# Optimization experiments

Hardware: AMD Instinct MI355X
Metric: run time of the kernel (lower is better)

## Reference

```python
import jax, jax.numpy as jnp
import numpy as np

EPS = 1e-5
B, L, D_MSA, D_PAIR = 1, 512, 256, 128
D_STATE, L0_IN, L0_OUT, EF = 32, 32, 32, 32
CV_IN, CV_OUT, C_HID = 3, 3, 32
TOP_K = 64
D_NODE_IN = D_MSA + 21 + D_STATE  # 309
D_INV = 2 * L0_IN + EF + 1 + CV_IN  # 100


def ln(x, g, b):
    mu = x.mean(-1, keepdims=True)
    var = ((x - mu) ** 2).mean(-1, keepdims=True)
    return (x - mu) * jax.lax.rsqrt(var + EPS) * g + b


def setup_inputs():
    key = jax.random.key(0)
    ks = iter(jax.random.split(key, 64))
    r = lambda *s: jax.random.normal(next(ks), s, jnp.float32)
    inp = {
        'xyz': r(B, L, 3, 3) * 3.0,
        'state': r(B, L, D_STATE),
        'atom_coor': r(B, L, 14, 3),
        'atom_feat': r(B, L, 14, 21),
        'msa': r(B, L, D_MSA),
        'pair': r(B, L, L, D_PAIR),
        'seq1hot': jax.random.uniform(next(ks), (B, L, 21)),
        'idx': jnp.arange(L, dtype=jnp.int32)[None].repeat(B, 0),
        'CA_atom_index': jax.random.randint(next(ks), (B, L), 0, 14),
        'top_k': TOP_K,
        # LayerNorm params
        'g_msa': jnp.ones(D_MSA), 'b_msa': jnp.zeros(D_MSA),
        'g_pair': jnp.ones(D_PAIR), 'b_pair': jnp.zeros(D_PAIR),
        'g_state': jnp.ones(D_STATE), 'b_state': jnp.zeros(D_STATE),
        'g_node': jnp.ones(L0_IN), 'b_node': jnp.zeros(L0_IN),
        'g_e1': jnp.ones(EF), 'b_e1': jnp.zeros(EF),
        # embeddings
        'Wx': r(D_NODE_IN, L0_IN) * 0.02, 'bx': jnp.zeros(L0_IN),
        'We1': r(D_PAIR, EF) * 0.02, 'be1': jnp.zeros(EF),
        # SE3-equivariant layer params
        'W1': r(D_INV, C_HID) * 0.1, 'b1': jnp.zeros(C_HID),
        'W2': r(L0_IN + C_HID, L0_OUT) * 0.1, 'b2': jnp.zeros(L0_OUT),
        'Wv': r(C_HID, 2 * CV_OUT) * 0.1,
        'Wvv': r(CV_IN, CV_OUT) * 0.3,
        'Wself': r(CV_IN, CV_OUT) * 0.3,
        # lddt head
        'Wl': r(L0_OUT, 1) * 0.1, 'bl': jnp.zeros(1),
    }
    return inp


def reference(xyz, state, atom_coor, atom_feat, msa, pair, seq1hot, idx,
              CA_atom_index, top_k, g_msa, b_msa, g_pair, b_pair, g_state,
              b_state, g_node, b_node, g_e1, b_e1, Wx, bx, We1, be1,
              W1, b1, W2, b2, Wv, Wvv, Wself, Wl, bl):
    Bb, Ll = msa.shape[:2]
    N = Bb * Ll
    # node / pair / state embeddings with fused LN+Linear chains
    node = ln(msa, g_msa, b_msa)
    pair_n = ln(pair, g_pair, b_pair)
    st = ln(state, g_state, b_state)
    node = jnp.concatenate([node, seq1hot, st], axis=-1)          # [B,L,309]
    node = ln(node @ Wx + bx, g_node, b_node)                      # [B,L,32]
    pair_e = ln(pair_n @ We1 + be1, g_e1, b_e1)                    # [B,L,L,32]

    # ---- make_graph_topk: kNN graph on CA coords ----
    CA = xyz[:, :, 1]                                              # [B,L,3]
    D = jnp.sqrt(jnp.sum((CA[:, :, None] - CA[:, None]) ** 2, -1) + 1e-8)
    D = D + 999.9 * jnp.eye(Ll, dtype=D.dtype)
    _, nbr = jax.lax.top_k(-D, top_k)                              # [B,L,k]
    src = jnp.repeat(jnp.arange(N), top_k)                         # [E]
    dst = (nbr + (jnp.arange(Bb) * Ll)[:, None, None]).reshape(-1) # [E]
    CAf = CA.reshape(N, 3)
    d_e = jax.lax.stop_gradient(CAf[dst] - CAf[src])               # [E,3] (detached as in torch)
    w_e = jnp.take_along_axis(pair_e.reshape(N, Ll, EF),
                              nbr.reshape(N, top_k, 1), axis=1).reshape(-1, EF)

    # ---- SE(3)-equivariant message passing (degree-0 + degree-1) ----
    l0 = node.reshape(N, -1)                                       # [N,32]
    v = (xyz - CA[:, :, None]).reshape(N, CV_IN, 3)                # [N,3,3]
    dn = jnp.linalg.norm(d_e, axis=-1, keepdims=True)              # [E,1]
    du = d_e / (dn + 1e-8)
    sv = jnp.einsum('eiv,ev->ei', v[src], du)                      # [E,3] invariants
    inv = jnp.concatenate([l0[src], l0[dst], w_e, dn, sv], -1)     # [E,100]
    m = jax.nn.gelu(inv @ W1 + b1)                                 # [E,32]
    agg = jax.ops.segment_sum(m, dst, num_segments=N)              # [N,32] scatter
    h_out = jnp.concatenate([l0, agg], -1) @ W2 + b2               # [N,32]
    coef = m @ Wv                                                  # [E,6]
    cd, cv = coef[:, :CV_OUT], coef[:, CV_OUT:]
    vproj = jnp.einsum('io,niv->nov', Wvv, v)                      # [N,3,3]
    vmsg = cd[:, :, None] * d_e[:, None] + cv[:, :, None] * vproj[src]
    v_agg = jax.ops.segment_sum(vmsg, dst, num_segments=N)         # [N,3,3]
    v_out = jnp.einsum('io,niv->nov', Wself, v) + v_agg            # [N,3,3]

    # ---- assemble refined coordinates ----
    state_o = h_out.reshape(Bb, Ll, -1)
    offset = v_out.reshape(Bb, Ll, -1, 3)
    CA_new = CA + offset[:, :, 1]
    CA_set = jnp.repeat(CA_new[:, :, None], 3, axis=2)
    CA_set = CA_set.at[:, 0:1].set(0.0)
    xyz_new = (offset + CA_set).reshape(Bb * Ll * 3, 3)
    lddt = jax.nn.sigmoid(ln(state_o, g_state, b_state) @ Wl + bl)
    return xyz_new, lddt
```

## Files before the change

### kernel.cpp

```cpp
#include <hip/hip_runtime.h>
#include <hip/hip_bf16.h>
#include <math.h>

typedef __hip_bfloat16 bf16;

__device__ __forceinline__ bool detect_bf16(const void* ones_vec) {
  return ((const unsigned int*)ones_vec)[0] == 0x3F803F80u;
}
__device__ __forceinline__ float ldf(const void* p, long idx, bool isb) {
  if (isb) return __bfloat162float(((const bf16*)p)[idx]);
  return ((const float*)p)[idx];
}
__device__ __forceinline__ void stf(void* p, long idx, float v, bool isb) {
  if (isb) ((bf16*)p)[idx] = __float2bfloat16(v);
  else     ((float*)p)[idx] = v;
}
__device__ __forceinline__ float wsum64(float x) {
#pragma unroll
  for (int off = 32; off > 0; off >>= 1) x += __shfl_xor(x, off, 64);
  return x;
}
__device__ __forceinline__ float wsum32(float x) {
#pragma unroll
  for (int off = 16; off > 0; off >>= 1) x += __shfl_xor(x, off, 64);
  return x;
}

__global__ __launch_bounds__(256) void k_node_topk(
    const void* __restrict__ xyz, const void* __restrict__ state,
    const void* __restrict__ msa, const void* __restrict__ seq1hot,
    const void* __restrict__ g_msa, const void* __restrict__ b_msa,
    const void* __restrict__ g_state, const void* __restrict__ b_state,
    const void* __restrict__ g_node, const void* __restrict__ b_node,
    const void* __restrict__ Wx, const void* __restrict__ bx,
    const void* __restrict__ Wvv,
    float* __restrict__ l0, float* __restrict__ CA, float* __restrict__ v,
    float* __restrict__ vproj, float* __restrict__ agg, float* __restrict__ v_agg,
    int* __restrict__ nbr)
{
  const bool isb = detect_bf16(g_msa);
  const int i = blockIdx.x;
  const int t = threadIdx.x;
  const int lane = t & 63, w = t >> 6;
  __shared__ float nin[312];
  __shared__ float wred[2][4];
  __shared__ float part[8][32];
  __shared__ float sxyz[9], sv9[9];
  __shared__ float cx[512], cy[512], cz[512];
  __shared__ unsigned long long key[512];

  for (int tt = t; tt < 512; tt += 256) {
    cx[tt] = ldf(xyz, tt * 9 + 3, isb);
    cy[tt] = ldf(xyz, tt * 9 + 4, isb);
    cz[tt] = ldf(xyz, tt * 9 + 5, isb);
  }

  float x = ldf(msa, i * 256 + t, isb);
  float s1 = wsum64(x), s2 = wsum64(x * x);
  if (lane == 0) { wred[0][w] = s1; wred[1][w] = s2; }
  if (t < 9) sxyz[t] = ldf(xyz, i * 9 + t, isb);
  __syncthreads();
  float S  = wred[0][0] + wred[0][1] + wred[0][2] + wred[0][3];
  float Sq = wred[1][0] + wred[1][1] + wred[1][2] + wred[1][3];
  float mu = S * (1.f / 256.f);
  float rs = rsqrtf(fmaxf(Sq * (1.f / 256.f) - mu * mu, 0.f) + 1e-5f);
  nin[t] = (x - mu) * rs * ldf(g_msa, t, isb) + ldf(b_msa, t, isb);
  if (t < 21) nin[256 + t] = ldf(seq1hot, i * 21 + t, isb);
  if (t < 3)  nin[309 + t] = 0.f;

  if (w == 0) {
    float sx  = (lane < 32) ? ldf(state, i * 32 + lane, isb) : 0.f;
    float Ss  = wsum64(sx), Ssq = wsum64(sx * sx);
    float mus = Ss * (1.f / 32.f);
    float rss = rsqrtf(fmaxf(Ssq * (1.f / 32.f) - mus * mus, 0.f) + 1e-5f);
    if (lane < 32)
      nin[277 + lane] = (sx - mus) * rss * ldf(g_state, lane, isb) + ldf(b_state, lane, isb);
  }
  __syncthreads();

  const int c = t & 31, g = t >> 5;
  float acc = 0.f;
  for (int f = g; f < 309; f += 8) acc += nin[f] * ldf(Wx, f * 32 + c, isb);
  part[g][c] = acc;

  float xi = cx[i], yi = cy[i], zi = cz[i];
  for (int tt = t; tt < 512; tt += 256) {
    float dx = cx[tt] - xi, dy = cy[tt] - yi, dz = cz[tt] - zi;
    float d2 = dx * dx + dy * dy + dz * dz;
    unsigned int bits = (tt == i) ? 0x7f800000u : __float_as_uint(d2);
    key[tt] = ((unsigned long long)bits << 32) | (unsigned int)tt;
  }
  __syncthreads();

  if (w == 0) {
    float a = 0.f;
    if (lane < 32) {
      a = ldf(bx, lane, isb);
#pragma unroll
      for (int gg = 0; gg < 8; ++gg) a += part[gg][lane];
    }
    float Sa = wsum32(a), Saq = wsum32(a * a);
    float mn = Sa * (1.f / 32.f);
    float rn = rsqrtf(fmaxf(Saq * (1.f / 32.f) - mn * mn, 0.f) + 1e-5f);
    if (lane < 32)
      l0[i * 32 + lane] = (a - mn) * rn * ldf(g_node, lane, isb) + ldf(b_node, lane, isb);
  } else if (w == 1) {
    if (lane < 3) CA[i * 3 + lane] = sxyz[3 + lane];
    if (lane < 9) {
      float vv = sxyz[lane] - sxyz[3 + lane % 3];
      v[i * 9 + lane] = vv;
      sv9[lane] = vv;
    }
    if (lane < 32) agg[i * 32 + lane] = 0.f;
  } else if (w == 2) {
    if (lane < 9) v_agg[i * 9 + lane] = 0.f;
  }
  __syncthreads();
  if (w == 1 && lane < 9) {
    int o = lane / 3, xc = lane % 3;
    float s = 0.f;
#pragma unroll
    for (int ii = 0; ii < 3; ++ii) s += ldf(Wvv, ii * 3 + o, isb) * sv9[ii * 3 + xc];
    vproj[i * 9 + lane] = s;
  }

  for (int k = 2; k <= 512; k <<= 1) {
    for (int j = k >> 1; j > 0; j >>= 1) {
      __syncthreads();
      int tt  = threadIdx.x;
      int i0 = ((tt & ~(j - 1)) << 1) | (tt & (j - 1));
      int i1 = i0 | j;
      bool up = ((i0 & k) == 0);
      unsigned long long a = key[i0], b = key[i1];
      if ((a > b) == up) { key[i0] = b; key[i1] = a; }
    }
  }
  __syncthreads();
  if (threadIdx.x < 64)
    nbr[i * 64 + threadIdx.x] = (int)(key[threadIdx.x] & 0xffffffffu);
}

__global__ __launch_bounds__(256) void k_edge(
    const void* __restrict__ pair,
    const void* __restrict__ g_pair, const void* __restrict__ b_pair,
    const void* __restrict__ We1, const void* __restrict__ be1,
    const void* __restrict__ g_e1, const void* __restrict__ b_e1,
    const void* __restrict__ W1, const void* __restrict__ b1,
    const void* __restrict__ Wv,
    const int* __restrict__ nbr,
    const float* __restrict__ l0, const float* __restrict__ CA,
    const float* __restrict__ v, const float* __restrict__ vproj,
    float* __restrict__ agg, float* __restrict__ v_agg)
{
  const bool isb = detect_bf16(g_pair);
  __shared__ float ped[4][128];
  __shared__ float sinv[4][104];
  __shared__ float sgeo[21];

  const int i    = blockIdx.x >> 1;
  const int half = blockIdx.x & 1;
  const int tid  = threadIdx.x;
  const int w = tid >> 6, lane = tid & 63;
  const int c = lane & 31, h = lane >> 5;

  if (tid < 3)  sgeo[tid] = CA[i * 3 + tid];
  else if (tid < 12) sgeo[tid] = v[i * 9 + (tid - 3)];
  else if (tid < 21) sgeo[tid] = vproj[i * 9 + (tid - 12)];

  float we1r[64];
#pragma unroll
  for (int t = 0; t < 64; ++t) we1r[t] = ldf(We1, (h * 64 + t) * 32 + c, isb);
  float w1r[52];
#pragma unroll
  for (int t = 0; t < 52; ++t) {
    int f = h * 52 + t;
    w1r[t] = (f < 100) ? ldf(W1, f * 32 + c, isb) : 0.f;
  }
  const float gp0 = ldf(g_pair, 2 * lane, isb),     gp1 = ldf(g_pair, 2 * lane + 1, isb);
  const float bp0 = ldf(b_pair, 2 * lane, isb),     bp1 = ldf(b_pair, 2 * lane + 1, isb);
  const float be1c = ldf(be1, c, isb), ge1c = ldf(g_e1, c, isb);
  const float bee1c = ldf(b_e1, c, isb), b1c = ldf(b1, c, isb);
  float wvr[6];
#pragma unroll
  for (int o = 0; o < 6; ++o) wvr[o] = ldf(Wv, c * 6 + o, isb);

  if (h == 0) {
    sinv[w][c] = l0[i * 32 + c];
    if (c < 4) sinv[w][100 + c] = 0.f;
  }
  __syncthreads();

  const float cai0 = sgeo[0], cai1 = sgeo[1], cai2 = sgeo[2];

  int jn = nbr[i * 64 + half * 32 + w];
  float np0, np1;
  {
    const size_t pb = ((size_t)(i * 512 + jn)) * 128;
    if (isb) {
      np0 = __bfloat162float(((const bf16*)pair)[pb + 2 * lane]);
      np1 = __bfloat162float(((const bf16*)pair)[pb + 2 * lane + 1]);
    } else {
      float2 pp = ((const float2*)pair)[(pb >> 1) + lane];
      np0 = pp.x; np1 = pp.y;
    }
  }
  float nlj  = l0[jn * 32 + c];
  float ncax = CA[jn * 3 + 0], ncay = CA[jn * 3 + 1], ncaz = CA[jn * 3 + 2];

#pragma unroll 1
  for (int step = 0; step < 8; ++step) {
    const int j = jn;
    const float p0 = np0, p1 = np1, lj = nlj;
    const float cax = ncax, cay = ncay, caz = ncaz;

    if (step < 7) {
      jn = nbr[i * 64 + half * 32 + (step + 1) * 4 + w];
      const size_t pb = ((size_t)(i * 512 + jn)) * 128;
      if (isb) {
        np0 = __bfloat162float(((const bf16*)pair)[pb + 2 * lane]);
        np1 = __bfloat162float(((const bf16*)pair)[pb + 2 * lane + 1]);
      } else {
        float2 pp = ((const float2*)pair)[(pb >> 1) + lane];
        np0 = pp.x; np1 = pp.y;
      }
      nlj  = l0[jn * 32 + c];
      ncax = CA[jn * 3 + 0]; ncay = CA[jn * 3 + 1]; ncaz = CA[jn * 3 + 2];
    }

    float S  = wsum64(p0 + p1);
    float Sq = wsum64(p0 * p0 + p1 * p1);
    float mu = S * (1.f / 128.f);
    float rs = rsqrtf(fmaxf(Sq * (1.f / 128.f) - mu * mu, 0.f) + 1e-5f);
    ped[w][2 * lane]     = (p0 - mu) * rs * gp0 + bp0;
    ped[w][2 * lane + 1] = (p1 - mu) * rs * gp1 + bp1;

    float acc = 0.f;
    {
      const float4* p4 = (const float4*)&ped[w][h * 64];
#pragma unroll
      for (int t = 0; t < 16; ++t) {
        float4 pv = p4[t];
        acc += pv.x * we1r[4 * t]     + pv.y * we1r[4 * t + 1]
             + pv.z * we1r[4 * t + 2] + pv.w * we1r[4 * t + 3];
      }
    }
    acc += __shfl_xor(acc, 32, 64);
    acc += be1c;
    float m2 = wsum32(acc) * (1.f / 32.f);
    float r2 = rsqrtf(fmaxf(wsum32(acc * acc) * (1.f / 32.f) - m2 * m2, 0.f) + 1e-5f);
    float we = (acc - m2) * r2 * ge1c + bee1c;

    float dex = cax - cai0, dey = cay - cai1, dez = caz - cai2;
    float dn  = sqrtf(dex * dex + dey * dey + dez * dez);
    float idn = 1.f / (dn + 1e-8f);
    float dux = dex * idn, duy = dey * idn, duz = dez * idn;

    if (h == 0) { sinv[w][32 + c] = lj; sinv[w][64 + c] = we; }
    if (lane == 0) {
      sinv[w][96] = dn;
      sinv[w][97] = sgeo[3] * dux + sgeo[4] * duy + sgeo[5] * duz;
      sinv[w][98] = sgeo[6] * dux + sgeo[7] * duy + sgeo[8] * duz;
      sinv[w][99] = sgeo[9] * dux + sgeo[10] * duy + sgeo[11] * duz;
    }

    float a1 = 0.f;
    {
      const float4* i4 = (const float4*)&sinv[w][h * 52];
#pragma unroll
      for (int t = 0; t < 13; ++t) {
        float4 iv = i4[t];
        a1 += iv.x * w1r[4 * t]     + iv.y * w1r[4 * t + 1]
            + iv.z * w1r[4 * t + 2] + iv.w * w1r[4 * t + 3];
      }
    }
    a1 += __shfl_xor(a1, 32, 64);
    a1 += b1c;
    float u  = 0.7978845608028654f * (a1 + 0.044715f * a1 * a1 * a1);
    float mm = 0.5f * a1 * (1.f + tanhf(u));

    if (h == 0) atomicAdd(&agg[j * 32 + c], mm);

    float co[6];
#pragma unroll
    for (int o = 0; o < 6; ++o) co[o] = wsum32(mm * wvr[o]);
    if (lane < 9) {
      int o = lane / 3, xx = lane % 3;
      float dcomp = (xx == 0) ? dex : ((xx == 1) ? dey : dez);
      atomicAdd(&v_agg[j * 9 + lane], co[o] * dcomp + co[3 + o] * sgeo[12 + o * 3 + xx]);
    }
  }
}

__global__ __launch_bounds__(64) void k_out(
    const float* __restrict__ l0, const float* __restrict__ agg,
    const float* __restrict__ v, const float* __restrict__ v_agg,
    const float* __restrict__ CA,
    const void* __restrict__ W2, const void* __restrict__ b2,
    const void* __restrict__ Wself,
    const void* __restrict__ g_state, const void* __restrict__ b_state,
    const void* __restrict__ Wl, const void* __restrict__ bl,
    void* __restrict__ out)
{
  const bool isb = detect_bf16(g_state);
  const int l = blockIdx.x;
  const int lane = threadIdx.x;
  const int c = lane & 31, h = lane >> 5;
  __shared__ float scat[64], soff[9];
  if (lane < 32) { scat[lane] = l0[l * 32 + lane]; scat[32 + lane] = agg[l * 32 + lane]; }
  __syncthreads();

  float acc = 0.f;
  {
    const int fb = h * 32;
    for (int f = 0; f < 32; ++f) acc += scat[fb + f] * ldf(W2, (fb + f) * 32 + c, isb);
  }
  acc += __shfl_xor(acc, 32, 64);
  acc += ldf(b2, c, isb);

  float mu = wsum32(acc) * (1.f / 32.f);
  float rs = rsqrtf(fmaxf(wsum32(acc * acc) * (1.f / 32.f) - mu * mu, 0.f) + 1e-5f);
  float hn = (acc - mu) * rs * ldf(g_state, c, isb) + ldf(b_state, c, isb);
  float pre = wsum32(hn * ldf(Wl, c, isb)) + ldf(bl, 0, isb);
  if (lane == 0) stf(out, 4608 + l, 1.f / (1.f + expf(-pre)), isb);

  if (lane < 9) {
    int o = lane / 3, xx = lane % 3;
    float s = v_agg[l * 9 + lane];
#pragma unroll
    for (int ii = 0; ii < 3; ++ii) s += ldf(Wself, ii * 3 + o, isb) * v[l * 9 + ii * 3 + xx];
    soff[lane] = s;
  }
  __syncthreads();
  if (lane < 9) {
    int xx = lane % 3;
    float add = (l == 0) ? 0.f : (CA[l * 3 + xx] + soff[3 + xx]);
    stf(out, l * 9 + lane, soff[lane] + add, isb);
  }
}

extern "C" void kernel_launch(void* const* d_in, const int* in_sizes, int n_in,
                              void* d_out, int out_size, void* d_ws, size_t ws_size,
                              hipStream_t stream) {
  (void)in_sizes; (void)n_in; (void)out_size; (void)ws_size;
  const void* xyz     = d_in[0];
  const void* state   = d_in[1];
  const void* msa     = d_in[4];
  const void* pair    = d_in[5];
  const void* seq1hot = d_in[6];
  const void* g_msa   = d_in[10];
  const void* b_msa   = d_in[11];
  const void* g_pair  = d_in[12];
  const void* b_pair  = d_in[13];
  const void* g_state = d_in[14];
  const void* b_state = d_in[15];
  const void* g_node  = d_in[16];
  const void* b_node  = d_in[17];
  const void* g_e1    = d_in[18];
  const void* b_e1    = d_in[19];
  const void* Wx      = d_in[20];
  const void* bx      = d_in[21];
  const void* We1     = d_in[22];
  const void* be1     = d_in[23];
  const void* W1      = d_in[24];
  const void* b1      = d_in[25];
  const void* W2      = d_in[26];
  const void* b2      = d_in[27];
  const void* Wv      = d_in[28];
  const void* Wvv     = d_in[29];
  const void* Wself   = d_in[30];
  const void* Wl      = d_in[31];
  const void* bl      = d_in[32];

  float* ws    = (float*)d_ws;
  float* l0    = ws;
  float* CA    = ws + 16384;
  float* v     = ws + 17920;
  float* vproj = ws + 22528;
  float* agg   = ws + 27136;
  float* v_agg = ws + 43520;
  int*   nbr   = (int*)(ws + 48128);

  hipLaunchKernelGGL(k_node_topk, dim3(512), dim3(256), 0, stream,
                     xyz, state, msa, seq1hot, g_msa, b_msa, g_state, b_state,
                     g_node, b_node, Wx, bx, Wvv, l0, CA, v, vproj, agg, v_agg, nbr);
  hipLaunchKernelGGL(k_edge, dim3(1024), dim3(256), 0, stream,
                     pair, g_pair, b_pair, We1, be1, g_e1, b_e1, W1, b1, Wv,
                     nbr, l0, CA, v, vproj, agg, v_agg);
  hipLaunchKernelGGL(k_out, dim3(512), dim3(64), 0, stream,
                     l0, agg, v, v_agg, CA, W2, b2, Wself, g_state, b_state, Wl, bl,
                     (void*)d_out);
}
```

Measured before the change: 307.4 us.

## Hoist per-node W1 term, move W1 weights to LDS, cut edge kernel registers

Computes the l0[src]·W1 contribution plus bias once per block, since it is constant across that node's edges, so the per-edge invariant vector shrinks from 100 to 68 entries. The remaining W1 rows move from per-thread registers into a padded shared-memory tile, and the Wv coefficient reductions are split across the two half-waves and exchanged with shuffles. Launch bounds now request 4 blocks per CU, and the dot-product loops use two accumulators. The aim is lower register pressure and higher occupancy. The cost is extra LDS reads per edge and possible spilling under the tighter register limit.

New measurement: 368.5 us. 1.2x slower.

```diff
diff --git a/kernel.cpp b/kernel.cpp
--- a/kernel.cpp
+++ b/kernel.cpp
@@ -140,7 +140,7 @@
     nbr[i * 64 + threadIdx.x] = (int)(key[threadIdx.x] & 0xffffffffu);
 }
 
-__global__ __launch_bounds__(256) void k_edge(
+__global__ __launch_bounds__(256, 4) void k_edge(
     const void* __restrict__ pair,
     const void* __restrict__ g_pair, const void* __restrict__ b_pair,
     const void* __restrict__ We1, const void* __restrict__ be1,
@@ -154,8 +154,9 @@
 {
   const bool isb = detect_bf16(g_pair);
   __shared__ float ped[4][128];
-  __shared__ float sinv[4][104];
+  __shared__ float sinv[4][72];
   __shared__ float sgeo[21];
+  __shared__ float W1L[32][76];
 
   const int i    = blockIdx.x >> 1;
   const int half = blockIdx.x & 1;
@@ -167,27 +168,32 @@
   else if (tid < 12) sgeo[tid] = v[i * 9 + (tid - 3)];
   else if (tid < 21) sgeo[tid] = vproj[i * 9 + (tid - 12)];
 
+  for (int idx = tid; idx < 32 * 72; idx += 256) {
+    int cc = idx & 31, t = idx >> 5;
+    W1L[cc][t] = (32 + t < 100) ? ldf(W1, (32 + t) * 32 + cc, isb) : 0.f;
+  }
+
   float we1r[64];
 #pragma unroll
   for (int t = 0; t < 64; ++t) we1r[t] = ldf(We1, (h * 64 + t) * 32 + c, isb);
-  float w1r[52];
-#pragma unroll
-  for (int t = 0; t < 52; ++t) {
-    int f = h * 52 + t;
-    w1r[t] = (f < 100) ? ldf(W1, f * 32 + c, isb) : 0.f;
-  }
   const float gp0 = ldf(g_pair, 2 * lane, isb),     gp1 = ldf(g_pair, 2 * lane + 1, isb);
   const float bp0 = ldf(b_pair, 2 * lane, isb),     bp1 = ldf(b_pair, 2 * lane + 1, isb);
   const float be1c = ldf(be1, c, isb), ge1c = ldf(g_e1, c, isb);
-  const float bee1c = ldf(b_e1, c, isb), b1c = ldf(b1, c, isb);
-  float wvr[6];
-#pragma unroll
-  for (int o = 0; o < 6; ++o) wvr[o] = ldf(Wv, c * 6 + o, isb);
-
-  if (h == 0) {
-    sinv[w][c] = l0[i * 32 + c];
-    if (c < 4) sinv[w][100 + c] = 0.f;
-  }
+  const float bee1c = ldf(b_e1, c, isb);
+  float wvr[3];
+#pragma unroll
+  for (int k = 0; k < 3; ++k) wvr[k] = ldf(Wv, c * 6 + 3 * h + k, isb);
+
+  float base = 0.f;
+#pragma unroll
+  for (int t = 0; t < 16; ++t) {
+    int f = h * 16 + t;
+    base += l0[i * 32 + f] * ldf(W1, f * 32 + c, isb);
+  }
+  base += __shfl_xor(base, 32, 64);
+  base += ldf(b1, c, isb);
+
+  if (h == 0 && c < 4) sinv[w][68 + c] = 0.f;
   __syncthreads();
 
   const float cai0 = sgeo[0], cai1 = sgeo[1], cai2 = sgeo[2];
@@ -234,16 +240,19 @@
     ped[w][2 * lane]     = (p0 - mu) * rs * gp0 + bp0;
     ped[w][2 * lane + 1] = (p1 - mu) * rs * gp1 + bp1;
 
-    float acc = 0.f;
+    float acc0 = 0.f, acc1 = 0.f;
     {
       const float4* p4 = (const float4*)&ped[w][h * 64];
 #pragma unroll
-      for (int t = 0; t < 16; ++t) {
-        float4 pv = p4[t];
-        acc += pv.x * we1r[4 * t]     + pv.y * we1r[4 * t + 1]
-             + pv.z * we1r[4 * t + 2] + pv.w * we1r[4 * t + 3];
+      for (int t = 0; t < 16; t += 2) {
+        float4 pa = p4[t], pb = p4[t + 1];
+        acc0 += pa.x * we1r[4 * t]     + pa.y * we1r[4 * t + 1]
+              + pa.z * we1r[4 * t + 2] + pa.w * we1r[4 * t + 3];
+        acc1 += pb.x * we1r[4 * t + 4] + pb.y * we1r[4 * t + 5]
+              + pb.z * we1r[4 * t + 6] + pb.w * we1r[4 * t + 7];
       }
     }
+    float acc = acc0 + acc1;
     acc += __shfl_xor(acc, 32, 64);
     acc += be1c;
     float m2 = wsum32(acc) * (1.f / 32.f);
@@ -255,38 +264,48 @@
     float idn = 1.f / (dn + 1e-8f);
     float dux = dex * idn, duy = dey * idn, duz = dez * idn;
 
-    if (h == 0) { sinv[w][32 + c] = lj; sinv[w][64 + c] = we; }
+    if (h == 0) { sinv[w][c] = lj; sinv[w][32 + c] = we; }
     if (lane == 0) {
-      sinv[w][96] = dn;
-      sinv[w][97] = sgeo[3] * dux + sgeo[4] * duy + sgeo[5] * duz;
-      sinv[w][98] = sgeo[6] * dux + sgeo[7] * duy + sgeo[8] * duz;
-      sinv[w][99] = sgeo[9] * dux + sgeo[10] * duy + sgeo[11] * duz;
-    }
-
-    float a1 = 0.f;
+      sinv[w][64] = dn;
+      sinv[w][65] = sgeo[3] * dux + sgeo[4] * duy + sgeo[5] * duz;
+      sinv[w][66] = sgeo[6] * dux + sgeo[7] * duy + sgeo[8] * duz;
+      sinv[w][67] = sgeo[9] * dux + sgeo[10] * duy + sgeo[11] * duz;
+    }
+
+    float b0a = 0.f, b1a = 0.f;
     {
-      const float4* i4 = (const float4*)&sinv[w][h * 52];
-#pragma unroll
-      for (int t = 0; t < 13; ++t) {
-        float4 iv = i4[t];
-        a1 += iv.x * w1r[4 * t]     + iv.y * w1r[4 * t + 1]
-            + iv.z * w1r[4 * t + 2] + iv.w * w1r[4 * t + 3];
+      const float4* i4 = (const float4*)&sinv[w][h * 36];
+      const float4* w4 = (const float4*)&W1L[c][h * 36];
+#pragma unroll
+      for (int t = 0; t < 8; t += 2) {
+        float4 ia = i4[t],     wa = w4[t];
+        float4 ib = i4[t + 1], wb = w4[t + 1];
+        b0a += ia.x * wa.x + ia.y * wa.y + ia.z * wa.z + ia.w * wa.w;
+        b1a += ib.x * wb.x + ib.y * wb.y + ib.z * wb.z + ib.w * wb.w;
       }
-    }
+      float4 ia = i4[8], wa = w4[8];
+      b0a += ia.x * wa.x + ia.y * wa.y + ia.z * wa.z + ia.w * wa.w;
+    }
+    float a1 = b0a + b1a;
     a1 += __shfl_xor(a1, 32, 64);
-    a1 += b1c;
+    a1 += base;
     float u  = 0.7978845608028654f * (a1 + 0.044715f * a1 * a1 * a1);
     float mm = 0.5f * a1 * (1.f + tanhf(u));
 
     if (h == 0) atomicAdd(&agg[j * 32 + c], mm);
 
-    float co[6];
-#pragma unroll
-    for (int o = 0; o < 6; ++o) co[o] = wsum32(mm * wvr[o]);
+    float co0 = wsum32(mm * wvr[0]);
+    float co1 = wsum32(mm * wvr[1]);
+    float co2 = wsum32(mm * wvr[2]);
+    float ct0 = __shfl(co0, (lane & 31) + 32, 64);
+    float ct1 = __shfl(co1, (lane & 31) + 32, 64);
+    float ct2 = __shfl(co2, (lane & 31) + 32, 64);
     if (lane < 9) {
       int o = lane / 3, xx = lane % 3;
       float dcomp = (xx == 0) ? dex : ((xx == 1) ? dey : dez);
-      atomicAdd(&v_agg[j * 9 + lane], co[o] * dcomp + co[3 + o] * sgeo[12 + o * 3 + xx]);
+      float cd = (o == 0) ? co0 : ((o == 1) ? co1 : co2);
+      float cv = (o == 0) ? ct0 : ((o == 1) ? ct1 : ct2);
+      atomicAdd(&v_agg[j * 9 + lane], cd * dcomp + cv * sgeo[12 + o * 3 + xx]);
     }
   }
 }
```

## Restructure edge kernel to stage weights in LDS and batch 16 edges per block

Applied to the files above, without the earlier changes.

The edge kernel now handles 16 edges per block across 2048 blocks instead of looping over 8 steps per wave. Weights We1 and W1 are staged into swizzled shared-memory tiles rather than held in large per-thread register arrays. Each thread computes two edges' outputs per channel, and the l0[src] part of the first MLP layer is precomputed once per block as a bias. The intent is to cut register pressure, raise occupancy and parallelism, and reuse weights across edges. The cost is more syncthreads and repeated weight staging in every block.

New measurement: 292.0 us. 5.0% less time.

```diff
diff --git a/kernel.cpp b/kernel.cpp
--- a/kernel.cpp
+++ b/kernel.cpp
@@ -153,141 +153,172 @@
     float* __restrict__ agg, float* __restrict__ v_agg)
 {
   const bool isb = detect_bf16(g_pair);
-  __shared__ float ped[4][128];
-  __shared__ float sinv[4][104];
+  __shared__ float WT[32][132];
+  __shared__ float ped[16][132];
+  __shared__ float sinvL[16][68];
+  __shared__ float mL[16][33];
+  __shared__ float coefL[16][8];
+  __shared__ float geoE[16][4];
+  __shared__ float gpl[128], bpl[128];
+  __shared__ float a1b[32];
   __shared__ float sgeo[21];
-
-  const int i    = blockIdx.x >> 1;
-  const int half = blockIdx.x & 1;
-  const int tid  = threadIdx.x;
-  const int w = tid >> 6, lane = tid & 63;
-  const int c = lane & 31, h = lane >> 5;
-
-  if (tid < 3)  sgeo[tid] = CA[i * 3 + tid];
-  else if (tid < 12) sgeo[tid] = v[i * 9 + (tid - 3)];
-  else if (tid < 21) sgeo[tid] = vproj[i * 9 + (tid - 12)];
-
-  float we1r[64];
-#pragma unroll
-  for (int t = 0; t < 64; ++t) we1r[t] = ldf(We1, (h * 64 + t) * 32 + c, isb);
-  float w1r[52];
-#pragma unroll
-  for (int t = 0; t < 52; ++t) {
-    int f = h * 52 + t;
-    w1r[t] = (f < 100) ? ldf(W1, f * 32 + c, isb) : 0.f;
-  }
-  const float gp0 = ldf(g_pair, 2 * lane, isb),     gp1 = ldf(g_pair, 2 * lane + 1, isb);
-  const float bp0 = ldf(b_pair, 2 * lane, isb),     bp1 = ldf(b_pair, 2 * lane + 1, isb);
-  const float be1c = ldf(be1, c, isb), ge1c = ldf(g_e1, c, isb);
-  const float bee1c = ldf(b_e1, c, isb), b1c = ldf(b1, c, isb);
-  float wvr[6];
-#pragma unroll
-  for (int o = 0; o < 6; ++o) wvr[o] = ldf(Wv, c * 6 + o, isb);
-
-  if (h == 0) {
-    sinv[w][c] = l0[i * 32 + c];
-    if (c < 4) sinv[w][100 + c] = 0.f;
-  }
-  __syncthreads();
-
-  const float cai0 = sgeo[0], cai1 = sgeo[1], cai2 = sgeo[2];
-
-  int jn = nbr[i * 64 + half * 32 + w];
-  float np0, np1;
-  {
-    const size_t pb = ((size_t)(i * 512 + jn)) * 128;
+  __shared__ float wvL[6][33];
+  __shared__ int   jnL[16];
+
+  const int i  = blockIdx.x >> 2;
+  const int qt = blockIdx.x & 3;
+  const int t  = threadIdx.x;
+  const int e  = t >> 4;
+  const int q  = t & 15;
+  const int c  = t & 31;
+  const int rg = t >> 5;
+
+  if (t < 16) jnL[t] = nbr[i * 64 + qt * 16 + t];
+  __syncthreads();
+
+  const int j_e = jnL[e];
+  float4 pA, pB;
+  {
+    const size_t base = ((size_t)(i * 512 + j_e)) * 128 + q * 8;
     if (isb) {
-      np0 = __bfloat162float(((const bf16*)pair)[pb + 2 * lane]);
-      np1 = __bfloat162float(((const bf16*)pair)[pb + 2 * lane + 1]);
+      pA.x = ldf(pair, base + 0, true); pA.y = ldf(pair, base + 1, true);
+      pA.z = ldf(pair, base + 2, true); pA.w = ldf(pair, base + 3, true);
+      pB.x = ldf(pair, base + 4, true); pB.y = ldf(pair, base + 5, true);
+      pB.z = ldf(pair, base + 6, true); pB.w = ldf(pair, base + 7, true);
     } else {
-      float2 pp = ((const float2*)pair)[(pb >> 1) + lane];
-      np0 = pp.x; np1 = pp.y;
+      const float4* p4 = (const float4*)pair;
+      pA = p4[base >> 2]; pB = p4[(base >> 2) + 1];
     }
   }
-  float nlj  = l0[jn * 32 + c];
-  float ncax = CA[jn * 3 + 0], ncay = CA[jn * 3 + 1], ncaz = CA[jn * 3 + 2];
-
-#pragma unroll 1
-  for (int step = 0; step < 8; ++step) {
-    const int j = jn;
-    const float p0 = np0, p1 = np1, lj = nlj;
-    const float cax = ncax, cay = ncay, caz = ncaz;
-
-    if (step < 7) {
-      jn = nbr[i * 64 + half * 32 + (step + 1) * 4 + w];
-      const size_t pb = ((size_t)(i * 512 + jn)) * 128;
-      if (isb) {
-        np0 = __bfloat162float(((const bf16*)pair)[pb + 2 * lane]);
-        np1 = __bfloat162float(((const bf16*)pair)[pb + 2 * lane + 1]);
-      } else {
-        float2 pp = ((const float2*)pair)[(pb >> 1) + lane];
-        np0 = pp.x; np1 = pp.y;
-      }
-      nlj  = l0[jn * 32 + c];
-      ncax = CA[jn * 3 + 0]; ncay = CA[jn * 3 + 1]; ncaz = CA[jn * 3 + 2];
-    }
-
-    float S  = wsum64(p0 + p1);
-    float Sq = wsum64(p0 * p0 + p1 * p1);
+
+  if (t < 128) gpl[t] = ldf(g_pair, t, isb);
+  else         bpl[t - 128] = ldf(b_pair, t - 128, isb);
+  for (int idx = t; idx < 4096; idx += 256) {
+    int cc = idx & 31, k = idx >> 5;
+    int slot = ((k >> 2) + 4 * (cc & 7)) & 31;
+    WT[cc][slot * 4 + (k & 3)] = ldf(We1, idx, isb);
+  }
+  {
+    int ee = t >> 4, kk = (t & 15) * 2;
+    const float2 lj = *(const float2*)&l0[jnL[ee] * 32 + kk];
+    sinvL[ee][kk] = lj.x; sinvL[ee][kk + 1] = lj.y;
+  }
+  if (t < 3)       sgeo[t] = CA[i * 3 + t];
+  else if (t < 12) sgeo[t] = v[i * 9 + (t - 3)];
+  else if (t < 21) sgeo[t] = vproj[i * 9 + (t - 12)];
+  if (t < 192) wvL[t % 6][t / 6] = ldf(Wv, t, isb);
+  if (t < 32) {
+    float b = ldf(b1, t, isb);
+    for (int f = 0; f < 32; ++f) b += l0[i * 32 + f] * ldf(W1, f * 32 + t, isb);
+    a1b[t] = b;
+  }
+
+  float S  = pA.x + pA.y + pA.z + pA.w + pB.x + pB.y + pB.z + pB.w;
+  float Sq = pA.x * pA.x + pA.y * pA.y + pA.z * pA.z + pA.w * pA.w
+           + pB.x * pB.x + pB.y * pB.y + pB.z * pB.z + pB.w * pB.w;
+#pragma unroll
+  for (int off = 8; off > 0; off >>= 1) {
+    S  += __shfl_xor(S,  off, 64);
+    Sq += __shfl_xor(Sq, off, 64);
+  }
+  __syncthreads();
+
+  {
     float mu = S * (1.f / 128.f);
     float rs = rsqrtf(fmaxf(Sq * (1.f / 128.f) - mu * mu, 0.f) + 1e-5f);
-    ped[w][2 * lane]     = (p0 - mu) * rs * gp0 + bp0;
-    ped[w][2 * lane + 1] = (p1 - mu) * rs * gp1 + bp1;
-
-    float acc = 0.f;
-    {
-      const float4* p4 = (const float4*)&ped[w][h * 64];
-#pragma unroll
-      for (int t = 0; t < 16; ++t) {
-        float4 pv = p4[t];
-        acc += pv.x * we1r[4 * t]     + pv.y * we1r[4 * t + 1]
-             + pv.z * we1r[4 * t + 2] + pv.w * we1r[4 * t + 3];
-      }
-    }
-    acc += __shfl_xor(acc, 32, 64);
-    acc += be1c;
-    float m2 = wsum32(acc) * (1.f / 32.f);
-    float r2 = rsqrtf(fmaxf(wsum32(acc * acc) * (1.f / 32.f) - m2 * m2, 0.f) + 1e-5f);
-    float we = (acc - m2) * r2 * ge1c + bee1c;
-
-    float dex = cax - cai0, dey = cay - cai1, dez = caz - cai2;
+    float4 g0 = *(const float4*)&gpl[q * 8], g1 = *(const float4*)&gpl[q * 8 + 4];
+    float4 b0 = *(const float4*)&bpl[q * 8], b1v = *(const float4*)&bpl[q * 8 + 4];
+    float4 o0, o1;
+    o0.x = (pA.x - mu) * rs * g0.x + b0.x;
+    o0.y = (pA.y - mu) * rs * g0.y + b0.y;
+    o0.z = (pA.z - mu) * rs * g0.z + b0.z;
+    o0.w = (pA.w - mu) * rs * g0.w + b0.w;
+    o1.x = (pB.x - mu) * rs * g1.x + b1v.x;
+    o1.y = (pB.y - mu) * rs * g1.y + b1v.y;
+    o1.z = (pB.z - mu) * rs * g1.z + b1v.z;
+    o1.w = (pB.w - mu) * rs * g1.w + b1v.w;
+    *(float4*)&ped[e][q * 8]     = o0;
+    *(float4*)&ped[e][q * 8 + 4] = o1;
+  }
+  if (t < 16) {
+    int j = jnL[t];
+    float dex = CA[j * 3 + 0] - sgeo[0];
+    float dey = CA[j * 3 + 1] - sgeo[1];
+    float dez = CA[j * 3 + 2] - sgeo[2];
     float dn  = sqrtf(dex * dex + dey * dey + dez * dez);
     float idn = 1.f / (dn + 1e-8f);
     float dux = dex * idn, duy = dey * idn, duz = dez * idn;
-
-    if (h == 0) { sinv[w][32 + c] = lj; sinv[w][64 + c] = we; }
-    if (lane == 0) {
-      sinv[w][96] = dn;
-      sinv[w][97] = sgeo[3] * dux + sgeo[4] * duy + sgeo[5] * duz;
-      sinv[w][98] = sgeo[6] * dux + sgeo[7] * duy + sgeo[8] * duz;
-      sinv[w][99] = sgeo[9] * dux + sgeo[10] * duy + sgeo[11] * duz;
+    sinvL[t][64] = dn;
+    sinvL[t][65] = sgeo[3] * dux + sgeo[4] * duy + sgeo[5] * duz;
+    sinvL[t][66] = sgeo[6] * dux + sgeo[7] * duy + sgeo[8] * duz;
+    sinvL[t][67] = sgeo[9] * dux + sgeo[10] * duy + sgeo[11] * duz;
+    geoE[t][0] = dex; geoE[t][1] = dey; geoE[t][2] = dez;
+  }
+  __syncthreads();
+
+  const int e0 = rg * 2, e1i = rg * 2 + 1;
+  const int rot = 4 * (c & 7);
+  float A0 = ldf(be1, c, isb), A1 = A0;
+#pragma unroll 4
+  for (int k4 = 0; k4 < 32; ++k4) {
+    float4 wf = *(const float4*)&WT[c][((k4 + rot) & 31) << 2];
+    float4 p0 = *(const float4*)&ped[e0][k4 << 2];
+    float4 p1 = *(const float4*)&ped[e1i][k4 << 2];
+    A0 += p0.x * wf.x + p0.y * wf.y + p0.z * wf.z + p0.w * wf.w;
+    A1 += p1.x * wf.x + p1.y * wf.y + p1.z * wf.z + p1.w * wf.w;
+  }
+  {
+    const float ge1c = ldf(g_e1, c, isb), bee1c = ldf(b_e1, c, isb);
+    float S0 = wsum32(A0), Q0 = wsum32(A0 * A0);
+    float S1 = wsum32(A1), Q1 = wsum32(A1 * A1);
+    float mu0 = S0 * (1.f / 32.f);
+    float r0  = rsqrtf(fmaxf(Q0 * (1.f / 32.f) - mu0 * mu0, 0.f) + 1e-5f);
+    float mu1 = S1 * (1.f / 32.f);
+    float r1  = rsqrtf(fmaxf(Q1 * (1.f / 32.f) - mu1 * mu1, 0.f) + 1e-5f);
+    sinvL[e0][32 + c]  = (A0 - mu0) * r0 * ge1c + bee1c;
+    sinvL[e1i][32 + c] = (A1 - mu1) * r1 * ge1c + bee1c;
+  }
+  __syncthreads();
+
+  for (int idx = t; idx < 2176; idx += 256) {
+    int cc = idx & 31, k = idx >> 5;
+    int slot = ((k >> 2) + 4 * (cc & 7)) & 31;
+    WT[cc][slot * 4 + (k & 3)] = ldf(W1, (32 + k) * 32 + cc, isb);
+  }
+  __syncthreads();
+
+  {
+    float M0 = a1b[c], M1 = M0;
+#pragma unroll 4
+    for (int k4 = 0; k4 < 17; ++k4) {
+      float4 wf = *(const float4*)&WT[c][((k4 + rot) & 31) << 2];
+      float4 s0 = *(const float4*)&sinvL[e0][k4 << 2];
+      float4 s1 = *(const float4*)&sinvL[e1i][k4 << 2];
+      M0 += s0.x * wf.x + s0.y * wf.y + s0.z * wf.z + s0.w * wf.w;
+      M1 += s1.x * wf.x + s1.y * wf.y + s1.z * wf.z + s1.w * wf.w;
     }
-
-    float a1 = 0.f;
-    {
-      const float4* i4 = (const float4*)&sinv[w][h * 52];
-#pragma unroll
-      for (int t = 0; t < 13; ++t) {
-        float4 iv = i4[t];
-        a1 += iv.x * w1r[4 * t]     + iv.y * w1r[4 * t + 1]
-            + iv.z * w1r[4 * t + 2] + iv.w * w1r[4 * t + 3];
-      }
-    }
-    a1 += __shfl_xor(a1, 32, 64);
-    a1 += b1c;
-    float u  = 0.7978845608028654f * (a1 + 0.044715f * a1 * a1 * a1);
-    float mm = 0.5f * a1 * (1.f + tanhf(u));
-
-    if (h == 0) atomicAdd(&agg[j * 32 + c], mm);
-
-    float co[6];
-#pragma unroll
-    for (int o = 0; o < 6; ++o) co[o] = wsum32(mm * wvr[o]);
-    if (lane < 9) {
-      int o = lane / 3, xx = lane % 3;
-      float dcomp = (xx == 0) ? dex : ((xx == 1) ? dey : dez);
-      atomicAdd(&v_agg[j * 9 + lane], co[o] * dcomp + co[3 + o] * sgeo[12 + o * 3 + xx]);
-    }
+    float u0 = 0.7978845608028654f * (M0 + 0.044715f * M0 * M0 * M0);
+    float g0 = 0.5f * M0 * (1.f + tanhf(u0));
+    float u1 = 0.7978845608028654f * (M1 + 0.044715f * M1 * M1 * M1);
+    float g1 = 0.5f * M1 * (1.f + tanhf(u1));
+    mL[e0][c] = g0;  mL[e1i][c] = g1;
+    atomicAdd(&agg[jnL[e0] * 32 + c], g0);
+    atomicAdd(&agg[jnL[e1i] * 32 + c], g1);
+  }
+  __syncthreads();
+
+  if (t < 96) {
+    int ee = t / 6, o = t - ee * 6;
+    float s = 0.f;
+#pragma unroll 8
+    for (int cc = 0; cc < 32; ++cc) s += mL[ee][cc] * wvL[o][cc];
+    coefL[ee][o] = s;
+  }
+  __syncthreads();
+  if (t < 144) {
+    int ee = t / 9, l = t - ee * 9, o = l / 3, x = l - o * 3;
+    float val = coefL[ee][o] * geoE[ee][x] + coefL[ee][3 + o] * sgeo[12 + o * 3 + x];
+    atomicAdd(&v_agg[jnL[ee] * 9 + l], val);
   }
 }
 
@@ -383,7 +414,7 @@
   hipLaunchKernelGGL(k_node_topk, dim3(512), dim3(256), 0, stream,
                      xyz, state, msa, seq1hot, g_msa, b_msa, g_state, b_state,
                      g_node, b_node, Wx, bx, Wvv, l0, CA, v, vproj, agg, v_agg, nbr);
-  hipLaunchKernelGGL(k_edge, dim3(1024), dim3(256), 0, stream,
+  hipLaunchKernelGGL(k_edge, dim3(2048), dim3(256), 0, stream,
                      pair, g_pair, b_pair, We1, be1, g_e1, b_e1, W1, b1, Wv,
                      nbr, l0, CA, v, vproj, agg, v_agg);
   hipLaunchKernelGGL(k_out, dim3(512), dim3(64), 0, stream,
```
